# Performance work log

Hardware: AMD Instinct MI355X
Metric: run time of the kernel (lower is better)

## Reference

```python
import jax, jax.numpy as jnp
import numpy as np

B, T, I, H, F = 32, 1024, 64, 512, 63
NEG = -1e9


def _init_params(key):
    ks = jax.random.split(key, 16)
    s = 0.02
    p = {}
    # LSTM (pytorch gate order i,f,g,o)
    p['w_ih'] = jax.random.normal(ks[0], (4 * H, I), jnp.float32) * s
    p['w_hh'] = jax.random.normal(ks[1], (4 * H, H), jnp.float32) * s
    p['b_ih'] = jnp.zeros((4 * H,), jnp.float32)
    p['b_hh'] = jnp.zeros((4 * H,), jnp.float32)
    # shared layer
    p['w_sh'] = jax.random.normal(ks[2], (H, H), jnp.float32) * s
    p['b_sh'] = jnp.zeros((H,), jnp.float32)
    # state attention: Linear(H,H) -> tanh -> Linear(H,1)
    p['w_sa'] = jax.random.normal(ks[3], (H, H), jnp.float32) * s
    p['b_sa'] = jnp.zeros((H,), jnp.float32)
    p['v_sa'] = jax.random.normal(ks[4], (1, H), jnp.float32) * s
    p['bv_sa'] = jnp.zeros((1,), jnp.float32)
    # reward attention
    p['w_ra'] = jax.random.normal(ks[5], (H, H), jnp.float32) * s
    p['b_ra'] = jnp.zeros((H,), jnp.float32)
    p['v_ra'] = jax.random.normal(ks[6], (1, H), jnp.float32) * s
    p['bv_ra'] = jnp.zeros((1,), jnp.float32)
    # heads
    p['w_st'] = jax.random.normal(ks[7], (F, H), jnp.float32) * s
    p['b_st'] = jnp.zeros((F,), jnp.float32)
    p['w_rw'] = jax.random.normal(ks[8], (1, H), jnp.float32) * s
    p['b_rw'] = jnp.zeros((1,), jnp.float32)
    return p


def setup_inputs() -> dict:
    key = jax.random.key(0)
    k1, k2, k3, kp = jax.random.split(key, 4)
    inp = {
        'x': jax.random.normal(k1, (B, T, I), jnp.float32),
        'x_lengths': jnp.full((B,), T, dtype=jnp.int64),  # full lengths: pack/pad is identity
        'h0': jax.random.normal(k2, (B, H), jnp.float32),
        'c0': jax.random.normal(k3, (B, H), jnp.float32),
    }
    inp.update(_init_params(kp))
    return inp


def _lstm(x, h0, c0, w_ih, w_hh, b_ih, b_hh):
    # x: [B,T,I] -> outputs [B,T,H], final (h,c)
    def step(carry, xt):
        h, c = carry
        gates = xt @ w_ih.T + h @ w_hh.T + b_ih + b_hh  # [B,4H]
        i, f, g, o = jnp.split(gates, 4, axis=-1)
        c = jax.nn.sigmoid(f) * c + jax.nn.sigmoid(i) * jnp.tanh(g)
        h = jax.nn.sigmoid(o) * jnp.tanh(c)
        return (h, c), h
    (hT, cT), outs = jax.lax.scan(step, (h0, c0), jnp.swapaxes(x, 0, 1))
    return jnp.swapaxes(outs, 0, 1), hT, cT


def _causal_attn(feat, w1, b1, v, bv):
    # additive attention pooling over every causal prefix, vectorized over t.
    e = jnp.tanh(feat @ w1.T + b1) @ v.T + bv        # [B,T,1]
    e = e[..., 0]                                     # [B,T]
    t = feat.shape[1]
    causal = jnp.tril(jnp.ones((t, t), bool))         # [T,T] j<=t
    logits = jnp.where(causal[None], e[:, None, :], NEG)
    w = jax.nn.softmax(logits, axis=-1)               # [B,T,T]
    return jnp.einsum('btj,bjh->bth', w, feat)        # [B,T,H]


def reference(x, x_lengths, h0, c0, w_ih, w_hh, b_ih, b_hh, w_sh, b_sh,
              w_sa, b_sa, v_sa, bv_sa, w_ra, b_ra, v_ra, bv_ra,
              w_st, b_st, w_rw, b_rw):
    r_out, hT, cT = _lstm(x, h0, c0, w_ih, w_hh, b_ih, b_hh)
    shared = r_out @ w_sh.T + b_sh                    # [B,T,H]
    state_ctx = _causal_attn(shared, w_sa, b_sa, v_sa, bv_sa)
    reward_ctx = _causal_attn(shared, w_ra, b_ra, v_ra, bv_ra)
    state_outs = state_ctx @ w_st.T + b_st            # [B,T,F]
    reward_outs = reward_ctx @ w_rw.T + b_rw          # [B,T,1]
    return state_outs, reward_outs, (hT, cT)
```

## Files before the change

kernel.cpp:

```cpp
#include <hip/hip_runtime.h>

#define BB 32
#define TT 1024
#define II 64
#define HH 512
#define FF 63
#define G4H 2048
#define KK 576
#define MM 32768
#define NW 32

#define RW_OFF 2064384
#define HT_OFF 2097152
#define CT_OFF 2113536

#define WS_FLAGS   0
#define WS_FLAG    4096
#define WS_TICK    4224
#define WS_CHOSEN  4288
#define WS_BIASC   8448
#define WS_BSH     16640
#define WS_BCSA    18688
#define WS_BCRA    20736
#define WS_BCH     22784
#define WS_SCAL    23040
#define WS_VS      23168
#define WS_VR      24192
#define WS_ZB      25216
#define WS_H0      27264
#define WS_CP      60032
#define WS_WHPAD   92800
#define WS_WHC     223872
#define WS_WSHT    354944
#define WS_WSA     879232
#define WS_WRA     1403520
#define WS_WCSA    1927808
#define WS_WCRA    2452096
#define WS_WCAT    2976384
#define WS_XP      5335680
#define WS_ES      9529984
#define WS_ER      9661056
#define WS_PROJ    9792128
#define WS_HX      13986432

typedef __bf16  bf16x8 __attribute__((ext_vector_type(8)));
typedef float   f32x4  __attribute__((ext_vector_type(4)));
typedef uint4 uint4a __attribute__((may_alias));
typedef unsigned int u32;

__device__ __forceinline__ float bf2f(unsigned short u) {
    unsigned int v = ((unsigned int)u) << 16;
    return __builtin_bit_cast(float, v);
}
__device__ __forceinline__ unsigned short f2bf(float f) {
    unsigned int u = __builtin_bit_cast(unsigned int, f);
    u += 0x7fffu + ((u >> 16) & 1u);
    return (unsigned short)(u >> 16);
}
__device__ __forceinline__ bf16x8 ldb8(const unsigned short* p) {
    uint4 v = *(const uint4a*)p;
    return __builtin_bit_cast(bf16x8, v);
}
__device__ __forceinline__ float sigf(float x) { return 1.f / (1.f + __expf(-x)); }
__device__ __forceinline__ float tanhfast(float x) { return 1.f - 2.f / (__expf(2.f * x) + 1.f); }

__device__ __forceinline__ unsigned short loadu(const void* p, int i, int fl) {
    return fl ? f2bf(((const float*)p)[i]) : ((const unsigned short*)p)[i];
}
__device__ __forceinline__ float loadf(const void* p, int i, int fl) {
    return fl ? ((const float*)p)[i] : bf2f(((const unsigned short*)p)[i]);
}

__global__ void sniff_k(const unsigned short* __restrict__ xr, unsigned int* __restrict__ flag) {
    if (threadIdx.x == 0) {
        int cnt = 0;
        for (int i = 0; i < 256; ++i) {
            unsigned short u = xr[i];
            int e = (u >> 7) & 0xFF;
            if (u == 0 || (e >= 100 && e <= 140)) ++cnt;
        }
        *flag = (cnt < 220) ? 1u : 0u;
    }
}

__global__ void prep_all(const void* x, const void* h0, const void* c0,
                         const void* w_sh, const void* w_sa, const void* w_ra,
                         const void* w_st, const void* w_rw,
                         const void* v_sa, const void* v_ra,
                         const void* b_sh, const void* bv_sa, const void* bv_ra,
                         char* ws) {
    const int fl = (int)*(const unsigned int*)(ws + WS_FLAG);
    unsigned short* xp    = (unsigned short*)(ws + WS_XP);
    unsigned short* h0s   = (unsigned short*)(ws + WS_H0);
    unsigned short* cp    = (unsigned short*)(ws + WS_CP);
    unsigned short* wshT  = (unsigned short*)(ws + WS_WSHT);
    unsigned short* wsa   = (unsigned short*)(ws + WS_WSA);
    unsigned short* wra   = (unsigned short*)(ws + WS_WRA);
    unsigned short* whpad = (unsigned short*)(ws + WS_WHPAD);
    unsigned short* vs    = (unsigned short*)(ws + WS_VS);
    unsigned short* vr    = (unsigned short*)(ws + WS_VR);
    float* bsh  = (float*)(ws + WS_BSH);
    float* scal = (float*)(ws + WS_SCAL);
    float* zb   = (float*)(ws + WS_ZB);

    int gt = blockIdx.x * 256 + threadIdx.x;
    int gs = gridDim.x * 256;
    for (int i = gt; i < BB * TT * II; i += gs) xp[i] = loadu(x, i, fl);
    for (int i = gt; i < BB * HH; i += gs) { h0s[i] = loadu(h0, i, fl); cp[i] = loadu(c0, i, fl); }
    for (int i = gt; i < HH * HH; i += gs) {
        int m = i >> 9, k = i & 511;
        wshT[i] = loadu(w_sh, k * HH + m, fl);
        wsa[i] = loadu(w_sa, i, fl);
        wra[i] = loadu(w_ra, i, fl);
    }
    for (int i = gt; i < 128 * HH; i += gs) {
        int f = i >> 9, k = i & 511;
        whpad[i] = (f < FF) ? loadu(w_st, f * HH + k, fl)
                 : (f == FF ? loadu(w_rw, k, fl) : (unsigned short)0);
    }
    for (int i = gt; i < HH; i += gs) {
        vs[i] = loadu(v_sa, i, fl); vr[i] = loadu(v_ra, i, fl);
        bsh[i] = loadf(b_sh, i, fl); zb[i] = 0.f;
    }
    if (gt == 0) { scal[0] = loadf(bv_sa, 0, fl); scal[1] = loadf(bv_ra, 0, fl); }
}

__global__ void prep_w(const void* __restrict__ w_hh, const void* __restrict__ w_ih,
                       const void* __restrict__ b_ih, const void* __restrict__ b_hh,
                       char* ws) {
    const int fl = (int)*(const unsigned int*)(ws + WS_FLAG);
    unsigned short* wcat = (unsigned short*)(ws + WS_WCAT);
    float* biasc = (float*)(ws + WS_BIASC);
    int c = blockIdx.x;
    for (int k = threadIdx.x; k < KK; k += 256)
        wcat[c * KK + k] = (k < HH) ? loadu(w_hh, c * HH + k, fl)
                                    : loadu(w_ih, c * II + (k - HH), fl);
    if (threadIdx.x == 0) biasc[c] = loadf(b_ih, c, fl) + loadf(b_hh, c, fl);
}

__global__ void bias_comb(const void* b_sa, const void* b_ra,
                          const void* b_st, const void* b_rw, char* ws) {
    const int fl = (int)*(const unsigned int*)(ws + WS_FLAG);
    const float* bsh = (const float*)(ws + WS_BSH);
    int j = threadIdx.x;
    if (blockIdx.x == 0) {
        const unsigned short* w = (const unsigned short*)(ws + WS_WSA);
        float s = loadf(b_sa, j, fl);
        for (int k = 0; k < HH; ++k) s += bf2f(w[j * HH + k]) * bsh[k];
        ((float*)(ws + WS_BCSA))[j] = s;
    } else if (blockIdx.x == 1) {
        const unsigned short* w = (const unsigned short*)(ws + WS_WRA);
        float s = loadf(b_ra, j, fl);
        for (int k = 0; k < HH; ++k) s += bf2f(w[j * HH + k]) * bsh[k];
        ((float*)(ws + WS_BCRA))[j] = s;
    } else if (j < 64) {
        const unsigned short* w = (const unsigned short*)(ws + WS_WHPAD);
        float s = (j < FF) ? loadf(b_st, j, fl) : loadf(b_rw, 0, fl);
        for (int k = 0; k < HH; ++k) s += bf2f(w[j * HH + k]) * bsh[k];
        ((float*)(ws + WS_BCH))[j] = s;
    }
}

__global__ __launch_bounds__(256, 1)
void lstm_k(char* __restrict__ ws, void* __restrict__ dout) {
    __shared__ float gbuf[32][68];
    __shared__ int s_slot;
    __shared__ u32 s_go;

    u32* tick   = (u32*)(ws + WS_TICK);
    u32* chosen = (u32*)(ws + WS_CHOSEN);

    if (threadIdx.x == 0) {
        u32 xcc;
        asm volatile("s_getreg_b32 %0, hwreg(HW_REG_XCC_ID)" : "=s"(xcc));
        xcc &= 7u;
        int slot = -1;
        u32 tk = __hip_atomic_fetch_add(&tick[xcc], 1u, __ATOMIC_RELAXED,
                                        __HIP_MEMORY_SCOPE_AGENT);
        if (tk < (u32)NW) {
            if (tk == (u32)NW - 1u) {
                u32 expected = 0u;
                __hip_atomic_compare_exchange_strong(chosen, &expected, xcc + 1u,
                    __ATOMIC_RELAXED, __ATOMIC_RELAXED, __HIP_MEMORY_SCOPE_AGENT);
            }
            u32 c = 0u;
            for (int it = 0; it < (1 << 20); ++it) {
                c = __hip_atomic_load(chosen, __ATOMIC_RELAXED, __HIP_MEMORY_SCOPE_AGENT);
                if (c != 0u) break;
                __builtin_amdgcn_s_sleep(8);
            }
            if (c == xcc + 1u) slot = (int)tk;
        }
        s_slot = slot;
        s_go = 0u;
    }
    __syncthreads();
    const int g = s_slot;
    if (g < 0) return;

    const unsigned short* xp    = (const unsigned short*)(ws + WS_XP);
    const unsigned short* wcat  = (const unsigned short*)(ws + WS_WCAT);
    const float*          biasc = (const float*)(ws + WS_BIASC);
    const unsigned short* cinit = (const unsigned short*)(ws + WS_CP);
    const unsigned short* h0s   = (const unsigned short*)(ws + WS_H0);
    unsigned short*       hx    = (unsigned short*)(ws + WS_HX);
    u32*                  flags = (u32*)(ws + WS_FLAGS);
    const int fl = (int)*(const unsigned int*)(ws + WS_FLAG);

    const int tid  = threadIdx.x;
    const int wave = tid >> 6, lane = tid & 63;
    const int quad = lane >> 4, l16 = lane & 15;
    const int mh = wave & 1, nh = wave >> 1;
    const int m = mh * 16 + l16;

    bf16x8 bw[2][18];
#pragma unroll
    for (int tn = 0; tn < 2; ++tn) {
        int nl   = nh * 32 + tn * 16 + l16;
        int gcol = (nl >> 4) * HH + g * 16 + (nl & 15);
        const unsigned short* wp = wcat + gcol * KK + quad * 8;
#pragma unroll
        for (int ks = 0; ks < 18; ++ks) bw[tn][ks] = ldb8(wp + ks * 32);
    }

    const int b  = tid >> 3, pr = tid & 7, cc = pr * 2;
    const int n  = g * 16 + cc;
    const float bi0 = biasc[n],          bi1 = biasc[n + 1];
    const float bff0 = biasc[HH + n],    bff1 = biasc[HH + n + 1];
    const float bg0 = biasc[2*HH + n],   bg1 = biasc[2*HH + n + 1];
    const float bo0 = biasc[3*HH + n],   bo1 = biasc[3*HH + n + 1];
    float cst0 = bf2f(cinit[b * HH + n]);
    float cst1 = bf2f(cinit[b * HH + n + 1]);

    const unsigned short* xbase = xp + m * (TT * II) + quad * 8;
    bf16x8 ax0 = ldb8(xbase), ax1 = ldb8(xbase + 32);

    u32* myflag = flags + g * 32;
    u32* pollp  = flags + (lane & 31) * 32;

    for (int t = 0; t < TT; ++t) {
        int tn1 = (t + 1 < TT) ? t + 1 : t;
        bf16x8 axn0 = ldb8(xbase + tn1 * II);
        bf16x8 axn1 = ldb8(xbase + tn1 * II + 32);

        const unsigned short* hrow =
            (t == 0 ? h0s : hx + (t - 1) * (BB * HH)) + m * HH + quad * 8;
        bf16x8 a[16];
#pragma unroll
        for (int i = 0; i < 16; ++i) a[i] = ldb8(hrow + i * 32);

        f32x4 acc0  = {0.f, 0.f, 0.f, 0.f}, acc1  = {0.f, 0.f, 0.f, 0.f};
        f32x4 acc0b = {0.f, 0.f, 0.f, 0.f}, acc1b = {0.f, 0.f, 0.f, 0.f};
        __builtin_amdgcn_s_setprio(1);
        acc0  = __builtin_amdgcn_mfma_f32_16x16x32_bf16(ax0, bw[0][16], acc0,  0, 0, 0);
        acc1  = __builtin_amdgcn_mfma_f32_16x16x32_bf16(ax0, bw[1][16], acc1,  0, 0, 0);
        acc0b = __builtin_amdgcn_mfma_f32_16x16x32_bf16(ax1, bw[0][17], acc0b, 0, 0, 0);
        acc1b = __builtin_amdgcn_mfma_f32_16x16x32_bf16(ax1, bw[1][17], acc1b, 0, 0, 0);
#pragma unroll
        for (int i = 0; i < 8; ++i) {
            acc0  = __builtin_amdgcn_mfma_f32_16x16x32_bf16(a[i],     bw[0][i],     acc0,  0, 0, 0);
            acc1  = __builtin_amdgcn_mfma_f32_16x16x32_bf16(a[i],     bw[1][i],     acc1,  0, 0, 0);
            acc0b = __builtin_amdgcn_mfma_f32_16x16x32_bf16(a[i + 8], bw[0][i + 8], acc0b, 0, 0, 0);
            acc1b = __builtin_amdgcn_mfma_f32_16x16x32_bf16(a[i + 8], bw[1][i + 8], acc1b, 0, 0, 0);
        }
        __builtin_amdgcn_s_setprio(0);
        acc0 = acc0 + acc0b;
        acc1 = acc1 + acc1b;

        {
            int row = mh * 16 + quad * 4;
#pragma unroll
            for (int r = 0; r < 4; ++r) gbuf[row + r][nh * 32 + l16]      = acc0[r];
#pragma unroll
            for (int r = 0; r < 4; ++r) gbuf[row + r][nh * 32 + 16 + l16] = acc1[r];
        }
        __syncthreads();

        {
            float2 giv = *(const float2*)&gbuf[b][cc];
            float2 gfv = *(const float2*)&gbuf[b][16 + cc];
            float2 ggv = *(const float2*)&gbuf[b][32 + cc];
            float2 gov = *(const float2*)&gbuf[b][48 + cc];
            cst0 = sigf(gfv.x + bff0) * cst0 + sigf(giv.x + bi0) * tanhfast(ggv.x + bg0);
            cst1 = sigf(gfv.y + bff1) * cst1 + sigf(giv.y + bi1) * tanhfast(ggv.y + bg1);
            float h0v = sigf(gov.x + bo0) * tanhfast(cst0);
            float h1v = sigf(gov.y + bo1) * tanhfast(cst1);
            u32 hp = (u32)f2bf(h0v) | ((u32)f2bf(h1v) << 16);
            *(u32*)&hx[t * (BB * HH) + b * HH + n] = hp;
            if (t == TT - 1) {
                if (fl) {
                    ((float*)dout)[HT_OFF + b * HH + n]     = h0v;
                    ((float*)dout)[HT_OFF + b * HH + n + 1] = h1v;
                    ((float*)dout)[CT_OFF + b * HH + n]     = cst0;
                    ((float*)dout)[CT_OFF + b * HH + n + 1] = cst1;
                } else {
                    ((u32*)dout)[(HT_OFF + b * HH + n) >> 1] = hp;
                    ((u32*)dout)[(CT_OFF + b * HH + n) >> 1] =
                        (u32)f2bf(cst0) | ((u32)f2bf(cst1) << 16);
                }
            }
        }
        __syncthreads();

        if (tid == 0)
            (void)__hip_atomic_fetch_add(myflag, 1u, __ATOMIC_RELAXED,
                                         __HIP_MEMORY_SCOPE_WORKGROUP);

        u32 die = 0u;
        if (wave == 0) {
            const u32 tgt = (u32)(t + 1);
            int it = 0;
            for (;;) {
                u32 v = (lane < 32)
                    ? __hip_atomic_load(pollp, __ATOMIC_RELAXED, __HIP_MEMORY_SCOPE_AGENT)
                    : tgt;
                if (__all((int)(v >= tgt))) break;
                if (++it > (1 << 17)) { die = 1u; break; }
            }
            if (lane == 0) {
                if (die)
                    __hip_atomic_store(myflag, (u32)(TT + 2), __ATOMIC_RELAXED,
                                       __HIP_MEMORY_SCOPE_AGENT);
                __hip_atomic_store(&s_go, die ? (u32)(TT + 2) : (u32)(t + 1),
                                   __ATOMIC_RELAXED, __HIP_MEMORY_SCOPE_WORKGROUP);
            }
        } else {
            const u32 tgt = (u32)(t + 1);
            int it = 0; u32 v;
            for (;;) {
                v = __hip_atomic_load(&s_go, __ATOMIC_RELAXED,
                                      __HIP_MEMORY_SCOPE_WORKGROUP);
                if (v >= tgt) break;
                if (++it > (1 << 21)) { v = (u32)(TT + 2); break; }
            }
            if (v >= (u32)(TT + 1)) die = 1u;
        }
        if (die) break;
        asm volatile("" ::: "memory");
        ax0 = axn0; ax1 = axn1;
    }
}

__global__ __launch_bounds__(256)
void gemm_bt(const unsigned short* __restrict__ A,
             const unsigned short* __restrict__ W,
             const float* __restrict__ bias,
             void* __restrict__ Cv, int N) {
    __shared__ unsigned short As[128][72];
    __shared__ unsigned short Bs[64][72];
    const int tid = threadIdx.x;
    const int wave = tid >> 6, lane = tid & 63, quad = lane >> 4, l16 = lane & 15;
    const int mb = blockIdx.x, nb = blockIdx.y;

    f32x4 acc[2][4];
#pragma unroll
    for (int tm = 0; tm < 2; ++tm)
#pragma unroll
        for (int tn = 0; tn < 4; ++tn) acc[tm][tn] = (f32x4){0.f, 0.f, 0.f, 0.f};

    for (int k0 = 0; k0 < 512; k0 += 64) {
#pragma unroll
        for (int i = 0; i < 4; ++i) {
            int v = tid + i * 256;
            int rowa = v >> 3, kc = (v & 7) * 8;
            *(uint4a*)&As[rowa][kc] = *(const uint4a*)(A + (mb * 128 + rowa) * 512 + k0 + kc);
        }
#pragma unroll
        for (int i = 0; i < 2; ++i) {
            int v = tid + i * 256;
            int rowb = v >> 3, kc = (v & 7) * 8;
            *(uint4a*)&Bs[rowb][kc] = *(const uint4a*)(W + (nb * 64 + rowb) * 512 + k0 + kc);
        }
        __syncthreads();
#pragma unroll
        for (int ks = 0; ks < 2; ++ks) {
            bf16x8 a0 = ldb8(&As[wave * 32 + l16][ks * 32 + quad * 8]);
            bf16x8 a1 = ldb8(&As[wave * 32 + 16 + l16][ks * 32 + quad * 8]);
#pragma unroll
            for (int tn = 0; tn < 4; ++tn) {
                bf16x8 bb = ldb8(&Bs[tn * 16 + l16][ks * 32 + quad * 8]);
                acc[0][tn] = __builtin_amdgcn_mfma_f32_16x16x32_bf16(a0, bb, acc[0][tn], 0, 0, 0);
                acc[1][tn] = __builtin_amdgcn_mfma_f32_16x16x32_bf16(a1, bb, acc[1][tn], 0, 0, 0);
            }
        }
        __syncthreads();
    }
#pragma unroll
    for (int tm = 0; tm < 2; ++tm)
#pragma unroll
        for (int tn = 0; tn < 4; ++tn)
#pragma unroll
            for (int r = 0; r < 4; ++r) {
                int row = mb * 128 + wave * 32 + tm * 16 + quad * 4 + r;
                int col = nb * 64 + tn * 16 + l16;
                ((unsigned short*)Cv)[row * N + col] = f2bf(acc[tm][tn][r] + bias[col]);
            }
}

__global__ __launch_bounds__(256)
void gemm_tail(const unsigned short* __restrict__ A,
               const unsigned short* __restrict__ Wes,
               const float* __restrict__ bes,
               const unsigned short* __restrict__ vvs,
               float* __restrict__ eout,
               const unsigned short* __restrict__ Wpj,
               const float* __restrict__ bpj,
               unsigned short* __restrict__ proj) {
    __shared__ unsigned short As[128][72];
    __shared__ unsigned short Bs[64][72];
    const int tid = threadIdx.x;
    const int wave = tid >> 6, lane = tid & 63, quad = lane >> 4, l16 = lane & 15;
    const int nb = blockIdx.x, mb = blockIdx.y;
    const bool ispj = (nb == 16);
    const unsigned short* W = ispj ? Wpj : (Wes + nb * 64 * 512);

    f32x4 acc[2][4];
#pragma unroll
    for (int tm = 0; tm < 2; ++tm)
#pragma unroll
        for (int tn = 0; tn < 4; ++tn) acc[tm][tn] = (f32x4){0.f, 0.f, 0.f, 0.f};

    for (int k0 = 0; k0 < 512; k0 += 64) {
#pragma unroll
        for (int i = 0; i < 4; ++i) {
            int v = tid + i * 256;
            int rowa = v >> 3, kc = (v & 7) * 8;
            *(uint4a*)&As[rowa][kc] = *(const uint4a*)(A + (mb * 128 + rowa) * 512 + k0 + kc);
        }
#pragma unroll
        for (int i = 0; i < 2; ++i) {
            int v = tid + i * 256;
            int rowb = v >> 3, kc = (v & 7) * 8;
            *(uint4a*)&Bs[rowb][kc] = *(const uint4a*)(W + rowb * 512 + k0 + kc);
        }
        __syncthreads();
#pragma unroll
        for (int ks = 0; ks < 2; ++ks) {
            bf16x8 a0 = ldb8(&As[wave * 32 + l16][ks * 32 + quad * 8]);
            bf16x8 a1 = ldb8(&As[wave * 32 + 16 + l16][ks * 32 + quad * 8]);
#pragma unroll
            for (int tn = 0; tn < 4; ++tn) {
                bf16x8 bb = ldb8(&Bs[tn * 16 + l16][ks * 32 + quad * 8]);
                acc[0][tn] = __builtin_amdgcn_mfma_f32_16x16x32_bf16(a0, bb, acc[0][tn], 0, 0, 0);
                acc[1][tn] = __builtin_amdgcn_mfma_f32_16x16x32_bf16(a1, bb, acc[1][tn], 0, 0, 0);
            }
        }
        __syncthreads();
    }
    if (ispj) {
#pragma unroll
        for (int tm = 0; tm < 2; ++tm)
#pragma unroll
            for (int tn = 0; tn < 4; ++tn)
#pragma unroll
                for (int r = 0; r < 4; ++r) {
                    int row = mb * 128 + wave * 32 + tm * 16 + quad * 4 + r;
                    int col = tn * 16 + l16;
                    proj[row * 64 + col] = f2bf(acc[tm][tn][r] + bpj[col]);
                }
    } else {
        const int eoff = (nb >= 8) ? MM : 0;
        float vcol[4], bcol[4];
#pragma unroll
        for (int tn = 0; tn < 4; ++tn) {
            int col = nb * 64 + tn * 16 + l16;
            vcol[tn] = bf2f(vvs[col]); bcol[tn] = bes[col];
        }
#pragma unroll
        for (int tm = 0; tm < 2; ++tm)
#pragma unroll
            for (int r = 0; r < 4; ++r) {
                float s = 0.f;
#pragma unroll
                for (int tn = 0; tn < 4; ++tn)
                    s += vcol[tn] * tanhfast(acc[tm][tn][r] + bcol[tn]);
                s += __shfl_xor(s, 1); s += __shfl_xor(s, 2);
                s += __shfl_xor(s, 4); s += __shfl_xor(s, 8);
                if (l16 == 0) {
                    int row = mb * 128 + wave * 32 + tm * 16 + quad * 4 + r;
                    atomicAdd(&eout[eoff + row], s);
                }
            }
    }
}

__global__ __launch_bounds__(64)
void cumsum_k(char* __restrict__ ws, void* __restrict__ dout) {
    const unsigned short* proj = (const unsigned short*)(ws + WS_PROJ);
    const float* es = (const float*)(ws + WS_ES);
    const float* er = (const float*)(ws + WS_ER);
    const float* scal = (const float*)(ws + WS_SCAL);
    const int fl = (int)*(const unsigned int*)(ws + WS_FLAG);
    const int b = blockIdx.x, lane = threadIdx.x;
    const bool isr = (lane == 63);
    const float bv = isr ? scal[1] : scal[0];
    float m_ = -3e38f, d_ = 0.f, n_ = 0.f;
    float pj = bf2f(proj[b * 64 + lane]);
    float e  = (isr ? er[b] : es[b]) + bv;
    for (int t = 0; t < TT; ++t) {
        float pjn = 0.f, en = 0.f;
        if (t + 1 < TT) {
            int rn = (t + 1) * BB + b;
            pjn = bf2f(proj[rn * 64 + lane]);
            en  = (isr ? er[rn] : es[rn]) + bv;
        }
        float mn = fmaxf(m_, e);
        float al = __expf(m_ - mn);
        float p  = __expf(e - mn);
        d_ = d_ * al + p;
        n_ = n_ * al + p * pj;
        m_ = mn;
        float o = n_ / d_;
        int rout = b * TT + t;
        int addr = isr ? (RW_OFF + rout) : (rout * FF + lane);
        if (fl) ((float*)dout)[addr] = o;
        else    ((unsigned short*)dout)[addr] = f2bf(o);
        pj = pjn; e = en;
    }
}

extern "C" void kernel_launch(void* const* d_in, const int* in_sizes, int n_in,
                              void* d_out, int out_size, void* d_ws, size_t ws_size,
                              hipStream_t stream) {
    const void* x    = d_in[0];
    const void* h0   = d_in[2];
    const void* c0   = d_in[3];
    const void* w_ih = d_in[4];
    const void* w_hh = d_in[5];
    const void* b_ih = d_in[6];
    const void* b_hh = d_in[7];
    const void* w_sh = d_in[8];
    const void* b_sh = d_in[9];
    const void* w_sa = d_in[10];
    const void* b_sa = d_in[11];
    const void* v_sa = d_in[12];
    const void* bv_sa= d_in[13];
    const void* w_ra = d_in[14];
    const void* b_ra = d_in[15];
    const void* v_ra = d_in[16];
    const void* bv_ra= d_in[17];
    const void* w_st = d_in[18];
    const void* b_st = d_in[19];
    const void* w_rw = d_in[20];
    const void* b_rw = d_in[21];

    char* ws = (char*)d_ws;
    unsigned short* wsa   = (unsigned short*)(ws + WS_WSA);
    unsigned short* whpad = (unsigned short*)(ws + WS_WHPAD);
    unsigned short* wshT  = (unsigned short*)(ws + WS_WSHT);
    unsigned short* wcsa  = (unsigned short*)(ws + WS_WCSA);
    unsigned short* whc   = (unsigned short*)(ws + WS_WHC);
    unsigned short* routs = (unsigned short*)(ws + WS_HX);
    unsigned short* proj  = (unsigned short*)(ws + WS_PROJ);
    unsigned short* vs    = (unsigned short*)(ws + WS_VS);
    float* zb   = (float*)(ws + WS_ZB);
    float* bcsa = (float*)(ws + WS_BCSA);
    float* bch  = (float*)(ws + WS_BCH);
    float* es   = (float*)(ws + WS_ES);

    (void)hipMemsetAsync(d_ws, 0, 8448, stream);
    (void)hipMemsetAsync(ws + WS_ES, 0, 2 * MM * 4, stream);
    sniff_k<<<1, 64, 0, stream>>>((const unsigned short*)x, (unsigned int*)(ws + WS_FLAG));
    prep_all<<<1024, 256, 0, stream>>>(x, h0, c0, w_sh, w_sa, w_ra, w_st, w_rw,
                                       v_sa, v_ra, b_sh, bv_sa, bv_ra, ws);
    prep_w<<<G4H, 256, 0, stream>>>(w_hh, w_ih, b_ih, b_hh, ws);

    lstm_k<<<256, 256, 0, stream>>>(ws, d_out);

    gemm_bt<<<dim3(8, 8), 256, 0, stream>>>(wsa,   wshT, zb, wcsa, 512);
    gemm_bt<<<dim3(1, 8), 256, 0, stream>>>(whpad, wshT, zb, whc,  512);
    bias_comb<<<3, 512, 0, stream>>>(b_sa, b_ra, b_st, b_rw, ws);

    gemm_tail<<<dim3(17, 256), 256, 0, stream>>>(routs, wcsa, bcsa, vs, es,
                                                 whc, bch, proj);
    cumsum_k<<<BB, 64, 0, stream>>>(ws, d_out);
}
```

Baseline: 4.056 ms.

## Split per-step LSTM barrier into two half-K waits so h-loads overlap sync

The single per-step wait on all 32 workgroups is replaced by two separate waits. One wave polls the 16 workgroups that produce the first half of h and another polls the other 16. The first half of the recurrent MFMAs starts as soon as its producers finish, so part of the cross-workgroup sync latency is hidden behind compute. The trailing __syncthreads is also dropped: each wave waits on its own stores with s_waitcnt and bumps the flag itself, so the flag targets become 4 per step. In exchange the protocol is more intricate, with relaxed atomics and per-wave flag increments, which raises the risk of visibility or ordering bugs and of dead-path handling mistakes.

```diff
diff --git a/kernel.cpp b/kernel.cpp
--- a/kernel.cpp
+++ b/kernel.cpp
@@ -165,7 +165,8 @@
 void lstm_k(char* __restrict__ ws, void* __restrict__ dout) {
     __shared__ float gbuf[32][68];
     __shared__ int s_slot;
-    __shared__ u32 s_go;
+    __shared__ u32 s_go_lo, s_go_hi;
+    __shared__ int s_dead;
 
     u32* tick   = (u32*)(ws + WS_TICK);
     u32* chosen = (u32*)(ws + WS_CHOSEN);
@@ -192,7 +193,8 @@
             if (c == xcc + 1u) slot = (int)tk;
         }
         s_slot = slot;
-        s_go = 0u;
+        s_go_lo = 0u; s_go_hi = 0u;
+        s_dead = 0;
     }
     __syncthreads();
     const int g = s_slot;
@@ -236,18 +238,31 @@
     bf16x8 ax0 = ldb8(xbase), ax1 = ldb8(xbase + 32);
 
     u32* myflag = flags + g * 32;
-    u32* pollp  = flags + (lane & 31) * 32;
+    u32* pollp  = flags + (((wave == 1) ? 16 : 0) + (lane & 15)) * 32;
 
     for (int t = 0; t < TT; ++t) {
         int tn1 = (t + 1 < TT) ? t + 1 : t;
         bf16x8 axn0 = ldb8(xbase + tn1 * II);
         bf16x8 axn1 = ldb8(xbase + tn1 * II + 32);
 
+        const u32 gt_ = (u32)t;
+        if (wave != 0) {
+            int it = 0; u32 v;
+            for (;;) {
+                v = __hip_atomic_load(&s_go_lo, __ATOMIC_RELAXED,
+                                      __HIP_MEMORY_SCOPE_WORKGROUP);
+                if (v >= gt_) break;
+                if (++it > (1 << 21)) { v = (u32)(TT + 2); break; }
+            }
+            if (v >= (u32)(TT + 1)) s_dead = 1;
+        }
+        asm volatile("" ::: "memory");
+
         const unsigned short* hrow =
             (t == 0 ? h0s : hx + (t - 1) * (BB * HH)) + m * HH + quad * 8;
-        bf16x8 a[16];
-#pragma unroll
-        for (int i = 0; i < 16; ++i) a[i] = ldb8(hrow + i * 32);
+        bf16x8 a[8];
+#pragma unroll
+        for (int i = 0; i < 8; ++i) a[i] = ldb8(hrow + i * 32);
 
         f32x4 acc0  = {0.f, 0.f, 0.f, 0.f}, acc1  = {0.f, 0.f, 0.f, 0.f};
         f32x4 acc0b = {0.f, 0.f, 0.f, 0.f}, acc1b = {0.f, 0.f, 0.f, 0.f};
@@ -258,10 +273,31 @@
         acc1b = __builtin_amdgcn_mfma_f32_16x16x32_bf16(ax1, bw[1][17], acc1b, 0, 0, 0);
 #pragma unroll
         for (int i = 0; i < 8; ++i) {
-            acc0  = __builtin_amdgcn_mfma_f32_16x16x32_bf16(a[i],     bw[0][i],     acc0,  0, 0, 0);
-            acc1  = __builtin_amdgcn_mfma_f32_16x16x32_bf16(a[i],     bw[1][i],     acc1,  0, 0, 0);
-            acc0b = __builtin_amdgcn_mfma_f32_16x16x32_bf16(a[i + 8], bw[0][i + 8], acc0b, 0, 0, 0);
-            acc1b = __builtin_amdgcn_mfma_f32_16x16x32_bf16(a[i + 8], bw[1][i + 8], acc1b, 0, 0, 0);
+            acc0 = __builtin_amdgcn_mfma_f32_16x16x32_bf16(a[i], bw[0][i], acc0, 0, 0, 0);
+            acc1 = __builtin_amdgcn_mfma_f32_16x16x32_bf16(a[i], bw[1][i], acc1, 0, 0, 0);
+        }
+        __builtin_amdgcn_s_setprio(0);
+
+        if (wave != 1) {
+            int it = 0; u32 v;
+            for (;;) {
+                v = __hip_atomic_load(&s_go_hi, __ATOMIC_RELAXED,
+                                      __HIP_MEMORY_SCOPE_WORKGROUP);
+                if (v >= gt_) break;
+                if (++it > (1 << 21)) { v = (u32)(TT + 2); break; }
+            }
+            if (v >= (u32)(TT + 1)) s_dead = 1;
+        }
+        asm volatile("" ::: "memory");
+
+        bf16x8 a2[8];
+#pragma unroll
+        for (int i = 0; i < 8; ++i) a2[i] = ldb8(hrow + (8 + i) * 32);
+        __builtin_amdgcn_s_setprio(1);
+#pragma unroll
+        for (int i = 0; i < 8; ++i) {
+            acc0b = __builtin_amdgcn_mfma_f32_16x16x32_bf16(a2[i], bw[0][8 + i], acc0b, 0, 0, 0);
+            acc1b = __builtin_amdgcn_mfma_f32_16x16x32_bf16(a2[i], bw[1][8 + i], acc1b, 0, 0, 0);
         }
         __builtin_amdgcn_s_setprio(0);
         acc0 = acc0 + acc0b;
@@ -275,6 +311,13 @@
             for (int r = 0; r < 4; ++r) gbuf[row + r][nh * 32 + 16 + l16] = acc1[r];
         }
         __syncthreads();
+
+        if (s_dead) {
+            if (tid == 0)
+                __hip_atomic_store(myflag, 0x0FFFFFFFu, __ATOMIC_RELAXED,
+                                   __HIP_MEMORY_SCOPE_AGENT);
+            break;
+        }
 
         {
             float2 giv = *(const float2*)&gbuf[b][cc];
@@ -300,42 +343,30 @@
                 }
             }
         }
-        __syncthreads();
-
-        if (tid == 0)
+
+        asm volatile("s_waitcnt vmcnt(0)" ::: "memory");
+        if (lane == 0)
             (void)__hip_atomic_fetch_add(myflag, 1u, __ATOMIC_RELAXED,
                                          __HIP_MEMORY_SCOPE_WORKGROUP);
 
-        u32 die = 0u;
-        if (wave == 0) {
-            const u32 tgt = (u32)(t + 1);
+        if (wave < 2) {
+            const u32 tgt = 4u * (u32)(t + 1);
+            u32 die = 0u;
             int it = 0;
             for (;;) {
-                u32 v = (lane < 32)
+                u32 v = (lane < 16)
                     ? __hip_atomic_load(pollp, __ATOMIC_RELAXED, __HIP_MEMORY_SCOPE_AGENT)
                     : tgt;
                 if (__all((int)(v >= tgt))) break;
                 if (++it > (1 << 17)) { die = 1u; break; }
             }
             if (lane == 0) {
-                if (die)
-                    __hip_atomic_store(myflag, (u32)(TT + 2), __ATOMIC_RELAXED,
-                                       __HIP_MEMORY_SCOPE_AGENT);
-                __hip_atomic_store(&s_go, die ? (u32)(TT + 2) : (u32)(t + 1),
+                u32* go = (wave == 0) ? &s_go_lo : &s_go_hi;
+                __hip_atomic_store(go, die ? (u32)(TT + 2) : (u32)(t + 1),
                                    __ATOMIC_RELAXED, __HIP_MEMORY_SCOPE_WORKGROUP);
-            }
-        } else {
-            const u32 tgt = (u32)(t + 1);
-            int it = 0; u32 v;
-            for (;;) {
-                v = __hip_atomic_load(&s_go, __ATOMIC_RELAXED,
-                                      __HIP_MEMORY_SCOPE_WORKGROUP);
-                if (v >= tgt) break;
-                if (++it > (1 << 21)) { v = (u32)(TT + 2); break; }
-            }
-            if (v >= (u32)(TT + 1)) die = 1u;
-        }
-        if (die) break;
+                if (die) s_dead = 1;
+            }
+        }
         asm volatile("" ::: "memory");
         ax0 = axn0; ax1 = axn1;
     }
```

New measurement: 4.407 ms. +8.6%, slower.

## Run weight-combination GEMMs in idle LSTM blocks to overlap with recurrence

Applied to the files above, without the earlier changes.

The LSTM kernel launches 256 blocks, but only 32 on one XCD do the recurrence and the rest used to exit at once. Those spare blocks now pull jobs from an atomic counter and compute the weight-combination GEMMs (W_sa·W_sh, head·W_sh) and the W·b_sh bias products while the recurrence runs. Two GEMM launches and the bias kernel are replaced by one small bias_fix kernel that adds the raw biases afterward. This saves launch overhead and serial time on work that is independent of the LSTM. The cost is extra shared memory in lstm_k and possible interference with the latency-bound recurrence blocks.

```diff
diff --git a/kernel.cpp b/kernel.cpp
--- a/kernel.cpp
+++ b/kernel.cpp
@@ -18,6 +18,7 @@
 #define WS_FLAG    4096
 #define WS_TICK    4224
 #define WS_CHOSEN  4288
+#define WS_TICK2   4352
 #define WS_BIASC   8448
 #define WS_BSH     16640
 #define WS_BCSA    18688
@@ -138,34 +139,14 @@
     if (threadIdx.x == 0) biasc[c] = loadf(b_ih, c, fl) + loadf(b_hh, c, fl);
 }
 
-__global__ void bias_comb(const void* b_sa, const void* b_ra,
-                          const void* b_st, const void* b_rw, char* ws) {
-    const int fl = (int)*(const unsigned int*)(ws + WS_FLAG);
-    const float* bsh = (const float*)(ws + WS_BSH);
-    int j = threadIdx.x;
-    if (blockIdx.x == 0) {
-        const unsigned short* w = (const unsigned short*)(ws + WS_WSA);
-        float s = loadf(b_sa, j, fl);
-        for (int k = 0; k < HH; ++k) s += bf2f(w[j * HH + k]) * bsh[k];
-        ((float*)(ws + WS_BCSA))[j] = s;
-    } else if (blockIdx.x == 1) {
-        const unsigned short* w = (const unsigned short*)(ws + WS_WRA);
-        float s = loadf(b_ra, j, fl);
-        for (int k = 0; k < HH; ++k) s += bf2f(w[j * HH + k]) * bsh[k];
-        ((float*)(ws + WS_BCRA))[j] = s;
-    } else if (j < 64) {
-        const unsigned short* w = (const unsigned short*)(ws + WS_WHPAD);
-        float s = (j < FF) ? loadf(b_st, j, fl) : loadf(b_rw, 0, fl);
-        for (int k = 0; k < HH; ++k) s += bf2f(w[j * HH + k]) * bsh[k];
-        ((float*)(ws + WS_BCH))[j] = s;
-    }
-}
-
 __global__ __launch_bounds__(256, 1)
 void lstm_k(char* __restrict__ ws, void* __restrict__ dout) {
     __shared__ float gbuf[32][68];
     __shared__ int s_slot;
     __shared__ u32 s_go;
+    __shared__ unsigned short As2[128][72];
+    __shared__ unsigned short Bs2[64][72];
+    __shared__ int s_job;
 
     u32* tick   = (u32*)(ws + WS_TICK);
     u32* chosen = (u32*)(ws + WS_CHOSEN);
@@ -196,7 +177,98 @@
     }
     __syncthreads();
     const int g = s_slot;
-    if (g < 0) return;
+
+    if (g < 0) {
+        const int tid = threadIdx.x;
+        const int wave = tid >> 6, lane = tid & 63;
+        const int quad = lane >> 4, l16 = lane & 15;
+        const unsigned short* wshT = (const unsigned short*)(ws + WS_WSHT);
+        const float* bsh = (const float*)(ws + WS_BSH);
+        for (;;) {
+            if (tid == 0)
+                s_job = (int)__hip_atomic_fetch_add((u32*)(ws + WS_TICK2), 1u,
+                            __ATOMIC_RELAXED, __HIP_MEMORY_SCOPE_AGENT);
+            __syncthreads();
+            const int job = s_job;
+            if (job >= 75) return;
+            if (job < 72) {
+                const int mb = (job < 64) ? (job >> 3) : 0;
+                const int nb = (job < 64) ? (job & 7) : (job - 64);
+                const unsigned short* A = (const unsigned short*)
+                    (ws + ((job < 64) ? WS_WSA : WS_WHPAD));
+                unsigned short* C = (unsigned short*)
+                    (ws + ((job < 64) ? WS_WCSA : WS_WHC));
+                f32x4 acc[2][4];
+#pragma unroll
+                for (int tm = 0; tm < 2; ++tm)
+#pragma unroll
+                    for (int tn = 0; tn < 4; ++tn) acc[tm][tn] = (f32x4){0.f, 0.f, 0.f, 0.f};
+                for (int k0 = 0; k0 < 512; k0 += 64) {
+#pragma unroll
+                    for (int i = 0; i < 4; ++i) {
+                        int v = tid + i * 256;
+                        int rowa = v >> 3, kc = (v & 7) * 8;
+                        *(uint4a*)&As2[rowa][kc] =
+                            *(const uint4a*)(A + (mb * 128 + rowa) * 512 + k0 + kc);
+                    }
+#pragma unroll
+                    for (int i = 0; i < 2; ++i) {
+                        int v = tid + i * 256;
+                        int rowb = v >> 3, kc = (v & 7) * 8;
+                        *(uint4a*)&Bs2[rowb][kc] =
+                            *(const uint4a*)(wshT + (nb * 64 + rowb) * 512 + k0 + kc);
+                    }
+                    __syncthreads();
+#pragma unroll
+                    for (int ks = 0; ks < 2; ++ks) {
+                        bf16x8 a0 = ldb8(&As2[wave * 32 + l16][ks * 32 + quad * 8]);
+                        bf16x8 a1 = ldb8(&As2[wave * 32 + 16 + l16][ks * 32 + quad * 8]);
+#pragma unroll
+                        for (int tn = 0; tn < 4; ++tn) {
+                            bf16x8 bb = ldb8(&Bs2[tn * 16 + l16][ks * 32 + quad * 8]);
+                            acc[0][tn] = __builtin_amdgcn_mfma_f32_16x16x32_bf16(a0, bb, acc[0][tn], 0, 0, 0);
+                            acc[1][tn] = __builtin_amdgcn_mfma_f32_16x16x32_bf16(a1, bb, acc[1][tn], 0, 0, 0);
+                        }
+                    }
+                    __syncthreads();
+                }
+#pragma unroll
+                for (int tm = 0; tm < 2; ++tm)
+#pragma unroll
+                    for (int tn = 0; tn < 4; ++tn)
+#pragma unroll
+                        for (int r = 0; r < 4; ++r) {
+                            int row = mb * 128 + wave * 32 + tm * 16 + quad * 4 + r;
+                            int col = nb * 64 + tn * 16 + l16;
+                            C[row * 512 + col] = f2bf(acc[tm][tn][r]);
+                        }
+            } else {
+                const int fl = (int)*(const unsigned int*)(ws + WS_FLAG);
+                if (job == 72 || job == 73) {
+                    const unsigned short* w = (const unsigned short*)
+                        (ws + ((job == 72) ? WS_WSA : WS_WRA));
+                    const char* b2 = (const char*)0;
+                    float* o = (float*)(ws + ((job == 72) ? WS_BCSA : WS_BCRA));
+                    (void)b2;
+                    for (int j = tid; j < 512; j += 256) {
+                        float s = (job == 72) ? ((float*)(ws + WS_SCAL))[0] * 0.f : 0.f;
+                        s = 0.f;
+                        for (int k = 0; k < HH; ++k) s += bf2f(w[j * HH + k]) * bsh[k];
+                        o[j] = s;
+                    }
+                } else {
+                    const unsigned short* w = (const unsigned short*)(ws + WS_WHPAD);
+                    float* o = (float*)(ws + WS_BCH);
+                    if (tid < 64) {
+                        float s = 0.f;
+                        for (int k = 0; k < HH; ++k) s += bf2f(w[tid * HH + k]) * bsh[k];
+                        o[tid] = s;
+                    }
+                }
+            }
+            __syncthreads();
+        }
+    }
 
     const unsigned short* xp    = (const unsigned short*)(ws + WS_XP);
     const unsigned short* wcat  = (const unsigned short*)(ws + WS_WCAT);
@@ -341,60 +413,14 @@
     }
 }
 
-__global__ __launch_bounds__(256)
-void gemm_bt(const unsigned short* __restrict__ A,
-             const unsigned short* __restrict__ W,
-             const float* __restrict__ bias,
-             void* __restrict__ Cv, int N) {
-    __shared__ unsigned short As[128][72];
-    __shared__ unsigned short Bs[64][72];
-    const int tid = threadIdx.x;
-    const int wave = tid >> 6, lane = tid & 63, quad = lane >> 4, l16 = lane & 15;
-    const int mb = blockIdx.x, nb = blockIdx.y;
-
-    f32x4 acc[2][4];
-#pragma unroll
-    for (int tm = 0; tm < 2; ++tm)
-#pragma unroll
-        for (int tn = 0; tn < 4; ++tn) acc[tm][tn] = (f32x4){0.f, 0.f, 0.f, 0.f};
-
-    for (int k0 = 0; k0 < 512; k0 += 64) {
-#pragma unroll
-        for (int i = 0; i < 4; ++i) {
-            int v = tid + i * 256;
-            int rowa = v >> 3, kc = (v & 7) * 8;
-            *(uint4a*)&As[rowa][kc] = *(const uint4a*)(A + (mb * 128 + rowa) * 512 + k0 + kc);
-        }
-#pragma unroll
-        for (int i = 0; i < 2; ++i) {
-            int v = tid + i * 256;
-            int rowb = v >> 3, kc = (v & 7) * 8;
-            *(uint4a*)&Bs[rowb][kc] = *(const uint4a*)(W + (nb * 64 + rowb) * 512 + k0 + kc);
-        }
-        __syncthreads();
-#pragma unroll
-        for (int ks = 0; ks < 2; ++ks) {
-            bf16x8 a0 = ldb8(&As[wave * 32 + l16][ks * 32 + quad * 8]);
-            bf16x8 a1 = ldb8(&As[wave * 32 + 16 + l16][ks * 32 + quad * 8]);
-#pragma unroll
-            for (int tn = 0; tn < 4; ++tn) {
-                bf16x8 bb = ldb8(&Bs[tn * 16 + l16][ks * 32 + quad * 8]);
-                acc[0][tn] = __builtin_amdgcn_mfma_f32_16x16x32_bf16(a0, bb, acc[0][tn], 0, 0, 0);
-                acc[1][tn] = __builtin_amdgcn_mfma_f32_16x16x32_bf16(a1, bb, acc[1][tn], 0, 0, 0);
-            }
-        }
-        __syncthreads();
-    }
-#pragma unroll
-    for (int tm = 0; tm < 2; ++tm)
-#pragma unroll
-        for (int tn = 0; tn < 4; ++tn)
-#pragma unroll
-            for (int r = 0; r < 4; ++r) {
-                int row = mb * 128 + wave * 32 + tm * 16 + quad * 4 + r;
-                int col = nb * 64 + tn * 16 + l16;
-                ((unsigned short*)Cv)[row * N + col] = f2bf(acc[tm][tn][r] + bias[col]);
-            }
+__global__ void bias_fix(const void* b_sa, const void* b_ra,
+                         const void* b_st, const void* b_rw, char* ws) {
+    const int fl = (int)*(const unsigned int*)(ws + WS_FLAG);
+    int j = threadIdx.x;
+    if (blockIdx.x == 0)      ((float*)(ws + WS_BCSA))[j] += loadf(b_sa, j, fl);
+    else if (blockIdx.x == 1) ((float*)(ws + WS_BCRA))[j] += loadf(b_ra, j, fl);
+    else if (j < 64)
+        ((float*)(ws + WS_BCH))[j] += (j < FF) ? loadf(b_st, j, fl) : loadf(b_rw, 0, fl);
 }
 
 __global__ __launch_bounds__(256)
@@ -545,15 +571,11 @@
     const void* b_rw = d_in[21];
 
     char* ws = (char*)d_ws;
-    unsigned short* wsa   = (unsigned short*)(ws + WS_WSA);
-    unsigned short* whpad = (unsigned short*)(ws + WS_WHPAD);
-    unsigned short* wshT  = (unsigned short*)(ws + WS_WSHT);
     unsigned short* wcsa  = (unsigned short*)(ws + WS_WCSA);
     unsigned short* whc   = (unsigned short*)(ws + WS_WHC);
     unsigned short* routs = (unsigned short*)(ws + WS_HX);
     unsigned short* proj  = (unsigned short*)(ws + WS_PROJ);
     unsigned short* vs    = (unsigned short*)(ws + WS_VS);
-    float* zb   = (float*)(ws + WS_ZB);
     float* bcsa = (float*)(ws + WS_BCSA);
     float* bch  = (float*)(ws + WS_BCH);
     float* es   = (float*)(ws + WS_ES);
@@ -567,9 +589,7 @@
 
     lstm_k<<<256, 256, 0, stream>>>(ws, d_out);
 
-    gemm_bt<<<dim3(8, 8), 256, 0, stream>>>(wsa,   wshT, zb, wcsa, 512);
-    gemm_bt<<<dim3(1, 8), 256, 0, stream>>>(whpad, wshT, zb, whc,  512);
-    bias_comb<<<3, 512, 0, stream>>>(b_sa, b_ra, b_st, b_rw, ws);
+    bias_fix<<<3, 512, 0, stream>>>(b_sa, b_ra, b_st, b_rw, ws);
 
     gemm_tail<<<dim3(17, 256), 256, 0, stream>>>(routs, wcsa, bcsa, vs, es,
                                                  whc, bch, proj);
```

Result: no change. 4.024 ms (-0.8%).
